# Performance work log

Measured on AMD Instinct MI355X. Metric: run time of the kernel, lower is better.

Reference implementation:

```python
import jax, jax.numpy as jnp
import numpy as np

NUM_PERSISTENT = 16
ALIBI_ALPHA = 1.0
START_I = 0
DILATION = 1
LN_EPS = 1e-5


def setup_inputs() -> dict:
    key = jax.random.key(0)
    ks = jax.random.split(key, 16)
    B, S, C, H = 8, 1024, 512, 8
    D = C // H
    P = NUM_PERSISTENT
    Kk = 3
    x = jax.random.normal(ks[0], (B, S, C), dtype=jnp.float32)
    mask = jnp.ones((B, 1, S, S), dtype=jnp.int32)
    sc = 0.02
    Wq = jax.random.normal(ks[1], (D, D), jnp.float32) * sc
    Wk = jax.random.normal(ks[2], (D, D), jnp.float32) * sc
    Wv = jax.random.normal(ks[3], (D, D), jnp.float32) * sc
    pk = jax.random.normal(ks[4], (P, H, D), jnp.float32) * sc
    pv = jax.random.normal(ks[5], (P, H, D), jnp.float32) * sc
    th_pre = jax.random.normal(ks[6], (H, H), jnp.float32) * (1.0 / np.sqrt(H))
    th_post = jax.random.normal(ks[7], (H, H), jnp.float32) * (1.0 / np.sqrt(H))
    fc_w = jax.random.normal(ks[8], (C, C), jnp.float32) * sc
    fc_b = jnp.zeros((C,), jnp.float32)
    conv1_w = jax.random.normal(ks[9], (C, C, Kk), jnp.float32) * 0.01
    conv1_b = jnp.zeros((C,), jnp.float32)
    conv2_w = jax.random.normal(ks[10], (C, C, Kk), jnp.float32) * 0.01
    conv2_b = jnp.zeros((C,), jnp.float32)
    ln_g = jnp.ones((C,), jnp.float32)
    ln_b = jnp.zeros((C,), jnp.float32)
    return dict(x=x, mask=mask, Wq=Wq, Wk=Wk, Wv=Wv, pk=pk, pv=pv,
                th_pre=th_pre, th_post=th_post, fc_w=fc_w, fc_b=fc_b,
                conv1_w=conv1_w, conv1_b=conv1_b, conv2_w=conv2_w,
                conv2_b=conv2_b, ln_g=ln_g, ln_b=ln_b)


def _causal_conv(x_nct, w_oik, b_o, dilation):
    # padding (k-1)*d on both sides + chomp right == pad left only
    k = w_oik.shape[-1]
    p = (k - 1) * dilation
    y = jax.lax.conv_general_dilated(
        x_nct, w_oik, window_strides=(1,), padding=[(p, 0)],
        rhs_dilation=(dilation,), dimension_numbers=("NCH", "OIH", "NCH"))
    return y + b_o[None, :, None]


def reference(x, mask, Wq, Wk, Wv, pk, pv, th_pre, th_post, fc_w, fc_b,
              conv1_w, conv1_b, conv2_w, conv2_b, ln_g, ln_b):
    N, S, C = x.shape
    H = th_pre.shape[0]
    D = C // H
    P = pk.shape[0]

    # ---- MultiHeadAttention (eval: dropout = identity) ----
    xh = x.reshape(N, S, H, D)
    q = jnp.einsum("nshd,ed->nshe", xh, Wq)
    k = jnp.einsum("nshd,ed->nshe", xh, Wk)
    v = jnp.einsum("nshd,ed->nshe", xh, Wv)
    # persistent memory tokens appended along key/value length
    k = jnp.concatenate([k, jnp.broadcast_to(pk[None], (N, P, H, D))], axis=1)
    v = jnp.concatenate([v, jnp.broadcast_to(pv[None], (N, P, H, D))], axis=1)

    energy = jnp.einsum("nqhd,nkhd->nhqk", q, k)  # (N,H,S,S+P)

    # ALiBi bias (symmetric |q-k|), zero over persistent keys
    slopes = 2.0 ** (-(ALIBI_ALPHA * (jnp.arange(1, H + 1, dtype=jnp.float32) + START_I)))
    t = jnp.arange(S, dtype=jnp.float32)
    dist = jnp.abs(t[:, None] - t[None, :])  # (S,S)
    bias = -dist[None, None] * slopes[None, :, None, None]  # (1,H,S,S)
    bias = jnp.pad(bias, ((0, 0), (0, 0), (0, 0), (0, P)))
    energy = energy + bias

    # pre-softmax talking heads (1x1 conv over head axis)
    energy = jnp.einsum("hg,ngqk->nhqk", th_pre, energy)

    ext_mask = jnp.pad(mask, ((0, 0), (0, 0), (0, 0), (0, P)), constant_values=1)
    energy = jnp.where(ext_mask == 0, jnp.float32(-1e4), energy)

    attn = jax.nn.softmax(energy / jnp.sqrt(jnp.float32(C)), axis=-1)
    attn = jnp.einsum("hg,ngqk->nhqk", th_post, attn)

    att_out = jnp.einsum("nhql,nlhd->nqhd", attn, v).reshape(N, S, C)
    att_out = att_out @ fc_w.T + fc_b

    x = x + att_out  # residual (dropout1 identity in eval)

    # ---- TemporalBlock (causal dilated convs, no SE since heads>0) ----
    xc = jnp.transpose(x, (0, 2, 1))  # (N,C,S)
    h = jax.nn.relu(_causal_conv(xc, conv1_w, conv1_b, DILATION))
    h = jax.nn.relu(_causal_conv(h, conv2_w, conv2_b, DILATION))
    out = jax.nn.relu(h + xc)  # downsample is None (in==out)

    # mask out invalid frames
    conv_mask = mask[:, 0, :, 0][:, None, :]  # (N,1,S)
    out = jnp.where(conv_mask == 0, 0.0, out)

    y = jnp.transpose(out, (0, 2, 1))  # (N,S,C)
    mu = jnp.mean(y, axis=-1, keepdims=True)
    var = jnp.mean(jnp.square(y - mu), axis=-1, keepdims=True)
    y = (y - mu) * jax.lax.rsqrt(var + LN_EPS) * ln_g + ln_b
    return y
```

## Files before the change

kernel.cpp:

```cpp
#include <hip/hip_runtime.h>
#include <hip/hip_bf16.h>

#define BN 8
#define SS 1024
#define CC 512
#define HH 8
#define DD 64
#define PP 16
#define KT 1040
#define KTE 1088

typedef __hip_bfloat16 bf16;
typedef unsigned char uchar;
typedef unsigned short ushort;
typedef unsigned int uint;
typedef __attribute__((ext_vector_type(8))) short short8;
typedef __attribute__((ext_vector_type(4))) float f32x4;
typedef __attribute__((ext_vector_type(2))) float f32x2;

__device__ __forceinline__ short f2s(float v){ bf16 b = __float2bfloat16(v); return *(short*)&b; }
__device__ __forceinline__ float s2f(short s){ bf16 b; *(short*)&b = s; return __bfloat162float(b); }
__device__ __forceinline__ uchar f2q(float v){
    return (uchar)__builtin_amdgcn_cvt_pk_fp8_f32(v, v, 0, false);
}
__device__ __forceinline__ float rfl(float x){
    return __int_as_float(__builtin_amdgcn_readfirstlane(__float_as_int(x)));
}

#define MFMA16(a,b,c)  __builtin_amdgcn_mfma_f32_16x16x32_bf16(a,b,c,0,0,0)
#define MFMAF8(a,b,c)  __builtin_amdgcn_mfma_f32_16x16x32_fp8_fp8(a,b,c,0,0,0)

__global__ __launch_bounds__(256) void prep_kernel(
    const float* __restrict__ fc_w, const float* __restrict__ c1w,
    const float* __restrict__ c2w, const float* __restrict__ Wq,
    const float* __restrict__ Wk, const float* __restrict__ Wv,
    const float* __restrict__ th_post,
    const float* __restrict__ pk, const float* __restrict__ pv,
    short* __restrict__ Bfc, uchar* __restrict__ Bc1,
    uchar* __restrict__ Bc2, short* __restrict__ Bqkv,
    uchar* __restrict__ kf, uchar* __restrict__ vt)
{
    int i = blockIdx.x*256 + threadIdx.x;
    const int NFC = 512*512, NCV = 512*1536, NQ = 3*64*64, NP = BN*HH*PP*DD;
    if (i < NFC) {
        int c = i >> 9, r = i & 511;
        int g = r >> 6, d = r & 63;
        float s = 0.f;
        #pragma unroll
        for (int h = 0; h < 8; ++h)
            s += fc_w[(size_t)c*512 + h*64 + d] * th_post[h*8 + g];
        Bfc[i] = f2s(s);
        return;
    }
    i -= NFC;
    if (i < NCV) {
        int o = i/1536, r = i%1536, dk = r>>9, ci = r&511;
        Bc1[i] = f2q(c1w[(o*512+ci)*3+dk] * 16.f); return;
    }
    i -= NCV;
    if (i < NCV) {
        int o = i/1536, r = i%1536, dk = r>>9, ci = r&511;
        Bc2[i] = f2q(c2w[(o*512+ci)*3+dk] * 16.f); return;
    }
    i -= NCV;
    if (i < NQ) {
        int w = i >> 12, rest = i & 4095;
        const float* W = (w==0)?Wq:(w==1)?Wk:Wv;
        Bqkv[i] = f2s(W[((rest>>6)&63)*64 + (rest&63)]);
        return;
    }
    i -= NQ;
    if (i < NP) {
        int d = i & 63, p = (i >> 6) & 15, h = (i >> 10) & 7, n = i >> 13;
        size_t src = ((size_t)p*HH + h)*DD + d;
        kf[(((size_t)(n*HH+h))*KT + SS + p)*DD + d] = f2q(pk[src]);
        vt[(((size_t)(n*HH+h))*DD + d)*KT + SS + p] = f2q(pv[src]);
    }
}

__global__ __launch_bounds__(256) void qkv_mfma(
    const float* __restrict__ x, const short* __restrict__ Bqkv,
    uchar* __restrict__ qf, uchar* __restrict__ kf, uchar* __restrict__ vt)
{
    __shared__ short Xs[64*72];
    __shared__ short Ws[192*72];
    const int tid = threadIdx.x;
    const int lin = blockIdx.x;
    const int xcd = lin & 7, slot = lin >> 3;
    const int m0 = (xcd*16 + (slot & 15))*64;
    const int h = slot >> 4;
    const int wave = tid >> 6, lane = tid & 63;
    const int lr = lane & 15, lq = lane >> 4;

    for (int i = tid; i < 1024; i += 256) {
        int r = i >> 4, cg = (i & 15)*4;
        float4 v = *(const float4*)(x + (size_t)(m0+r)*CC + h*64 + cg);
        Xs[r*72+cg+0] = f2s(v.x); Xs[r*72+cg+1] = f2s(v.y);
        Xs[r*72+cg+2] = f2s(v.z); Xs[r*72+cg+3] = f2s(v.w);
    }
    for (int i = tid; i < 3072; i += 256) {
        int r = i >> 4, cg = (i & 15)*4;
        *(short4*)(Ws + r*72 + cg) = *(const short4*)(Bqkv + (size_t)r*64 + cg);
    }
    __syncthreads();

    f32x4 acc[12];
    #pragma unroll
    for (int nt = 0; nt < 12; ++nt) acc[nt] = {0.f,0.f,0.f,0.f};
    #pragma unroll
    for (int ks = 0; ks < 2; ++ks) {
        int ko = ks*32 + lq*8;
        short8 a = *(const short8*)(Xs + (wave*16 + lr)*72 + ko);
        #pragma unroll
        for (int nt = 0; nt < 12; ++nt) {
            short8 b = *(const short8*)(Ws + (nt*16 + lr)*72 + ko);
            acc[nt] = MFMA16(a, b, acc[nt]);
        }
    }
    #pragma unroll
    for (int nt = 0; nt < 12; ++nt) {
        int ep = nt*16 + lr;
        int w = ep >> 6, e = ep & 63;
        #pragma unroll
        for (int reg = 0; reg < 4; ++reg) {
            int m = m0 + wave*16 + lq*4 + reg;
            int n = m >> 10, s = m & 1023;
            float v = acc[nt][reg];
            if (w == 0)      qf[((size_t)(n*HH+h)*SS + s)*DD + e] = f2q(v);
            else if (w == 1) kf[((size_t)(n*HH+h)*KT + s)*DD + e] = f2q(v);
            else             vt[(((size_t)(n*HH+h))*DD + e)*KT + s] = f2q(v);
        }
    }
}

__device__ __forceinline__ void en_loadK(const uchar* __restrict__ kf,
    int nh, int kt, int tid, uint2* rk)
{
    #pragma unroll
    for (int j = 0; j < 2; ++j) {
        int i = tid + j*256;
        int r = i >> 3, c8 = (i & 7)*8;
        int kcol = kt*64 + r;
        uint2 v = {0u, 0u};
        if (kcol < KT)
            v = *(const uint2*)(kf + ((size_t)nh*KT + kcol)*DD + c8);
        rk[j] = v;
    }
}

__global__ __launch_bounds__(256) void energy_mfma8(
    const uchar* __restrict__ qf, const uchar* __restrict__ kf,
    uchar* __restrict__ E)
{
    __shared__ uchar Qs[64*72];
    __shared__ uchar Ks[64*72];
    const int tid = threadIdx.x;
    const int lin = blockIdx.x + 16*blockIdx.y;
    const int xcd = lin & 7, slot = lin >> 3;
    const int nh = xcd*8 + (slot & 7);
    const int mt = slot >> 3;
    const int wave = tid >> 6, lane = tid & 63;
    const int lr = lane & 15, lq = lane >> 4;
    const int n = nh >> 3, h = nh & 7;

    #pragma unroll
    for (int j = 0; j < 2; ++j) {
        int i = tid + j*256;
        int r = i >> 3, c8 = (i & 7)*8;
        *(uint2*)(Qs + r*72 + c8) =
            *(const uint2*)(qf + ((size_t)nh*SS + mt*64 + r)*DD + c8);
    }

    uint2 rk[2];
    en_loadK(kf, nh, 0, tid, rk);

    for (int kt = 0; kt < 17; ++kt) {
        if (kt) __syncthreads();
        #pragma unroll
        for (int j = 0; j < 2; ++j) {
            int i = tid + j*256;
            *(uint2*)(Ks + (i >> 3)*72 + (i & 7)*8) = rk[j];
        }
        __syncthreads();
        if (kt + 1 < 17) en_loadK(kf, nh, kt+1, tid, rk);

        f32x4 acc[4];
        #pragma unroll
        for (int nt = 0; nt < 4; ++nt) acc[nt] = {0.f,0.f,0.f,0.f};
        #pragma unroll
        for (int ks = 0; ks < 2; ++ks) {
            int ko = ks*32 + lq*8;
            long a = *(const long*)(Qs + (wave*16 + lr)*72 + ko);
            #pragma unroll
            for (int nt = 0; nt < 4; ++nt) {
                long b = *(const long*)(Ks + (nt*16 + lr)*72 + ko);
                acc[nt] = MFMAF8(a, b, acc[nt]);
            }
        }
        #pragma unroll
        for (int nt = 0; nt < 4; ++nt) {
            int kcol = kt*64 + nt*16 + lr;
            if (kcol >= KT) continue;
            #pragma unroll
            for (int reg = 0; reg < 4; ++reg) {
                int q = mt*64 + wave*16 + lq*4 + reg;
                E[(((size_t)(n*SS + q))*HH + h)*KTE + kcol] = f2q(acc[nt][reg]);
            }
        }
    }
}

__global__ __launch_bounds__(256, 2) void pv_fused(
    const uchar* __restrict__ E, const uchar* __restrict__ vt,
    const int* __restrict__ mask, const float* __restrict__ th_pre,
    short* __restrict__ AO)
{
    __shared__ uchar Ps[4*16*72];
    __shared__ float Sred[16][4];
    const int tid  = threadIdx.x;
    const int n    = blockIdx.x;
    const int yy   = blockIdx.y;
    const int ql0  = (yy >> 1) * 16;
    const int hg   = (yy & 1) * 4;
    const int wave = tid >> 6, lane = tid & 63;
    const int h    = hg + wave;
    const int lr = lane & 15, lq = lane >> 4;
    const int q_l = lane >> 2, kc = lane & 3;
    const int q  = ql0 + q_l;
    const int kcol0 = kc*16;

    const float sc = 0.044194173824159216f * 1.4426950408889634f;
    float tw[8], slmix, shf;
    {
        const float slv[8] = {0.5f,0.25f,0.125f,0.0625f,
                              0.03125f,0.015625f,0.0078125f,0.00390625f};
        const float maxd = (float)((q > SS-1-q) ? q : (SS-1-q));
        float sm = 0.f;
        #pragma unroll
        for (int g = 0; g < 8; ++g) {
            float v = rfl(th_pre[h*8+g] * sc);
            tw[g] = v;
            sm += v * slv[g];
        }
        slmix = rfl(sm);
        shf = fmaxf(0.f, -slmix * maxd);
    }

    const uchar* Eb  = E  + ((size_t)(n*SS + q))*HH*KTE;
    const uchar* Vh  = vt + ((size_t)(n*HH) + h)*DD*KT;
    const int*  mrow = mask + (size_t)n*SS*SS + (size_t)q*SS;
    uchar* Psh = Ps + wave*1152;

    float sums = 0.f;
    f32x4 acc[4];
    #pragma unroll
    for (int j = 0; j < 4; ++j) acc[j] = {0.f,0.f,0.f,0.f};

    for (int kt = 0; kt < 17; ++kt) {
        const int kb = kt*64;
        const bool body = (kt < 16);

        uint4 rE[8];
        #pragma unroll
        for (int g = 0; g < 8; ++g)
            rE[g] = *(const uint4*)(Eb + (size_t)g*KTE + kb + kcol0);
        long bva[2][4];
        #pragma unroll
        for (int ks = 0; ks < 2; ++ks)
            #pragma unroll
            for (int nt = 0; nt < 4; ++nt)
                bva[ks][nt] = *(const long*)(Vh + (size_t)(nt*16+lr)*KT + kb + ks*32 + lq*8);
        int4 rm[4];
        if (body) {
            #pragma unroll
            for (int j = 0; j < 4; ++j)
                rm[j] = *(const int4*)(mrow + kb + kcol0 + j*4);
        }

        #pragma unroll
        for (int s = 0; s < 2; ++s) {
            const int k0 = kb + kcol0 + s*8;
            const bool valid = (k0 < KT);
            f32x4 tA, tB;
            if (body) {
                const float qv = (float)q, kf0 = (float)k0;
                f32x4 dA, dB;
                dA.x = fabsf(qv-kf0);      dA.y = fabsf(qv-kf0-1.f);
                dA.z = fabsf(qv-kf0-2.f);  dA.w = fabsf(qv-kf0-3.f);
                dB.x = fabsf(qv-kf0-4.f);  dB.y = fabsf(qv-kf0-5.f);
                dB.z = fabsf(qv-kf0-6.f);  dB.w = fabsf(qv-kf0-7.f);
                tA = -dA*slmix - shf;
                tB = -dB*slmix - shf;
            } else {
                tA = {-shf,-shf,-shf,-shf};
                tB = tA;
            }
            #pragma unroll
            for (int g = 0; g < 8; ++g) {
                const uint w0 = (s == 0) ? rE[g].x : rE[g].z;
                const uint w1 = (s == 0) ? rE[g].y : rE[g].w;
                f32x2 lo0 = __builtin_amdgcn_cvt_pk_f32_fp8((int)w0, false);
                f32x2 hi0 = __builtin_amdgcn_cvt_pk_f32_fp8((int)w0, true);
                f32x2 lo1 = __builtin_amdgcn_cvt_pk_f32_fp8((int)w1, false);
                f32x2 hi1 = __builtin_amdgcn_cvt_pk_f32_fp8((int)w1, true);
                f32x4 aA; aA.x=lo0.x; aA.y=lo0.y; aA.z=hi0.x; aA.w=hi0.y;
                f32x4 aB; aB.x=lo1.x; aB.y=lo1.y; aB.z=hi1.x; aB.w=hi1.y;
                tA += aA * tw[g];
                tB += aB * tw[g];
            }
            f32x4 eA, eB;
            if (body) {
                const int4 rmA = rm[2*s], rmB = rm[2*s+1];
                eA.x = (rmA.x==0)?0.f:exp2f(tA.x);
                eA.y = (rmA.y==0)?0.f:exp2f(tA.y);
                eA.z = (rmA.z==0)?0.f:exp2f(tA.z);
                eA.w = (rmA.w==0)?0.f:exp2f(tA.w);
                eB.x = (rmB.x==0)?0.f:exp2f(tB.x);
                eB.y = (rmB.y==0)?0.f:exp2f(tB.y);
                eB.z = (rmB.z==0)?0.f:exp2f(tB.z);
                eB.w = (rmB.w==0)?0.f:exp2f(tB.w);
            } else if (valid) {
                eA.x = exp2f(tA.x); eA.y = exp2f(tA.y);
                eA.z = exp2f(tA.z); eA.w = exp2f(tA.w);
                eB.x = exp2f(tB.x); eB.y = exp2f(tB.y);
                eB.z = exp2f(tB.z); eB.w = exp2f(tB.w);
            } else {
                eA = {0.f,0.f,0.f,0.f}; eB = {0.f,0.f,0.f,0.f};
            }
            sums += (eA.x+eA.y)+(eA.z+eA.w) + (eB.x+eB.y)+(eB.z+eB.w);
            int p0 = __builtin_amdgcn_cvt_pk_fp8_f32(eA.x, eA.y, 0, false);
            p0 = __builtin_amdgcn_cvt_pk_fp8_f32(eA.z, eA.w, p0, true);
            int p1 = __builtin_amdgcn_cvt_pk_fp8_f32(eB.x, eB.y, 0, false);
            p1 = __builtin_amdgcn_cvt_pk_fp8_f32(eB.z, eB.w, p1, true);
            uint2 pw; pw.x = (uint)p0; pw.y = (uint)p1;
            *(uint2*)(Psh + q_l*72 + kcol0 + s*8) = pw;
        }

        #pragma unroll
        for (int ks = 0; ks < 2; ++ks) {
            int ko = ks*32 + lq*8;
            long av = *(const long*)(Psh + lr*72 + ko);
            #pragma unroll
            for (int nt = 0; nt < 4; ++nt)
                acc[nt] = MFMAF8(av, bva[ks][nt], acc[nt]);
        }
    }

    {
        float s = sums;
        s += __shfl_xor(s, 1); s += __shfl_xor(s, 2);
        if (kc == 0) Sred[q_l][wave] = 1.0f / s;
    }

    #pragma unroll
    for (int reg = 0; reg < 4; ++reg) {
        float inv = Sred[lq*4 + reg][wave];
        int qg = ql0 + lq*4 + reg;
        #pragma unroll
        for (int nt = 0; nt < 4; ++nt) {
            int d = nt*16 + lr;
            AO[((size_t)(n*SS) + qg)*CC + h*64 + d] = f2s(acc[nt][reg] * inv);
        }
    }
}

__device__ __forceinline__ void g_load4(const short* __restrict__ src,
    size_t rowstride, int row0, int col0, int tid, short4* r)
{
    #pragma unroll
    for (int j = 0; j < 4; ++j) {
        int i = tid + j*256;
        int rr = i >> 4, cg = (i & 15)*4;
        r[j] = *(const short4*)(src + (size_t)(row0 + rr)*rowstride + col0 + cg);
    }
}
__device__ __forceinline__ void lds_store4(short* __restrict__ dst,
    int tid, const short4* r)
{
    #pragma unroll
    for (int j = 0; j < 4; ++j) {
        int i = tid + j*256;
        *(short4*)(dst + (i >> 4)*72 + (i & 15)*4) = r[j];
    }
}

__global__ __launch_bounds__(256) void fc_mfma(
    const short* __restrict__ A, const short* __restrict__ Bt,
    const float* __restrict__ bias, const float* __restrict__ x,
    short* __restrict__ out, uchar* __restrict__ out8)
{
    __shared__ short As[64*72];
    __shared__ short Bs[64*72];
    const int tid = threadIdx.x;
    const int lin = blockIdx.x + 8*blockIdx.y;
    const int xcd = lin & 7, slot = lin >> 3;
    const int m0 = (xcd*16 + (slot & 15))*64;
    const int n0 = (slot >> 4)*64;
    const int wave = tid >> 6, lane = tid & 63;
    const int lr = lane & 15, lq = lane >> 4;

    short4 ra[4], rb[4];
    g_load4(A, CC, m0, 0, tid, ra);
    g_load4(Bt, CC, n0, 0, tid, rb);

    f32x4 acc[4];
    #pragma unroll
    for (int nt = 0; nt < 4; ++nt) acc[nt] = {0.f,0.f,0.f,0.f};

    for (int kt = 0; kt < CC; kt += 64) {
        if (kt) __syncthreads();
        lds_store4(As, tid, ra);
        lds_store4(Bs, tid, rb);
        __syncthreads();
        if (kt + 64 < CC) {
            g_load4(A, CC, m0, kt+64, tid, ra);
            g_load4(Bt, CC, n0, kt+64, tid, rb);
        }
        #pragma unroll
        for (int ks = 0; ks < 2; ++ks) {
            int ko = ks*32 + lq*8;
            short8 a = *(const short8*)(As + (wave*16 + lr)*72 + ko);
            #pragma unroll
            for (int nt = 0; nt < 4; ++nt) {
                short8 b = *(const short8*)(Bs + (nt*16 + lr)*72 + ko);
                acc[nt] = MFMA16(a, b, acc[nt]);
            }
        }
    }
    #pragma unroll
    for (int nt = 0; nt < 4; ++nt) {
        int nn = n0 + nt*16 + lr;
        #pragma unroll
        for (int reg = 0; reg < 4; ++reg) {
            int m = m0 + wave*16 + lq*4 + reg;
            float v = acc[nt][reg] + bias[nn] + x[(size_t)m*CC + nn];
            out[(size_t)m*CC + nn]  = f2s(v);
            out8[(size_t)m*CC + nn] = f2q(v);
        }
    }
}

__device__ __forceinline__ void conv_loadA8w(const uchar* __restrict__ A,
    int m0, int kt, int tid, uint2* ra)
{
    const int shift = (kt >> 9) - 2;
    const int ci0 = kt & 511;
    #pragma unroll
    for (int j = 0; j < 4; ++j) {
        int i = tid + j*256;
        int rr = i >> 4, c8 = (i & 15)*8;
        int m = m0 + rr;
        int s = m & (SS-1);
        uint2 v = {0u, 0u};
        if (s + shift >= 0)
            v = *(const uint2*)(A + (size_t)(m + shift)*CC + ci0 + c8);
        ra[j] = v;
    }
}
__device__ __forceinline__ void g_load8w(const uchar* __restrict__ src,
    size_t rowstride, int row0, int col0, int tid, uint2* r)
{
    #pragma unroll
    for (int j = 0; j < 4; ++j) {
        int i = tid + j*256;
        int rr = i >> 4, c8 = (i & 15)*8;
        r[j] = *(const uint2*)(src + (size_t)(row0 + rr)*rowstride + col0 + c8);
    }
}
__device__ __forceinline__ void lds_store8w(uchar* __restrict__ dst,
    int tid, const uint2* r)
{
    #pragma unroll
    for (int j = 0; j < 4; ++j) {
        int i = tid + j*256;
        *(uint2*)(dst + (i >> 4)*136 + (i & 15)*8) = r[j];
    }
}

__global__ __launch_bounds__(256) void conv_mfma8(
    const uchar* __restrict__ A, const uchar* __restrict__ Bt,
    const float* __restrict__ bias, uchar* __restrict__ out8,
    short* __restrict__ out16, int f8out)
{
    __shared__ uchar As[64*136];
    __shared__ uchar Bs[64*136];
    const int tid = threadIdx.x;
    const int lin = blockIdx.x + 8*blockIdx.y;
    const int xcd = lin & 7, slot = lin >> 3;
    const int m0 = (xcd*16 + (slot & 15))*64;
    const int n0 = (slot >> 4)*64;
    const int wave = tid >> 6, lane = tid & 63;
    const int lr = lane & 15, lq = lane >> 4;

    uint2 ra[4], rb[4];
    conv_loadA8w(A, m0, 0, tid, ra);
    g_load8w(Bt, 1536, n0, 0, tid, rb);

    f32x4 acc[4];
    #pragma unroll
    for (int nt = 0; nt < 4; ++nt) acc[nt] = {0.f,0.f,0.f,0.f};

    for (int kt = 0; kt < 1536; kt += 128) {
        if (kt) __syncthreads();
        lds_store8w(As, tid, ra);
        lds_store8w(Bs, tid, rb);
        __syncthreads();
        if (kt + 128 < 1536) {
            conv_loadA8w(A, m0, kt+128, tid, ra);
            g_load8w(Bt, 1536, n0, kt+128, tid, rb);
        }
        #pragma unroll
        for (int ks = 0; ks < 4; ++ks) {
            int ko = ks*32 + lq*8;
            long a = *(const long*)(As + (wave*16 + lr)*136 + ko);
            #pragma unroll
            for (int nt = 0; nt < 4; ++nt) {
                long b = *(const long*)(Bs + (nt*16 + lr)*136 + ko);
                acc[nt] = MFMAF8(a, b, acc[nt]);
            }
        }
    }
    #pragma unroll
    for (int nt = 0; nt < 4; ++nt) {
        int nn = n0 + nt*16 + lr;
        #pragma unroll
        for (int reg = 0; reg < 4; ++reg) {
            int m = m0 + wave*16 + lq*4 + reg;
            float v = fmaxf(acc[nt][reg]*0.0625f + bias[nn], 0.f);
            if (f8out) out8[(size_t)m*CC + nn]  = f2q(v);
            else       out16[(size_t)m*CC + nn] = f2s(v);
        }
    }
}

__global__ __launch_bounds__(256) void final_kernel(
    const short* __restrict__ c2, const short* __restrict__ xres,
    const int* __restrict__ mask, const float* __restrict__ g,
    const float* __restrict__ b, float* __restrict__ out)
{
    __shared__ float red[256];
    const int tid = threadIdx.x;
    const int m0 = blockIdx.x * 4;
    const int c0 = tid*2;
    const float2 gg = *(const float2*)(g + c0);
    const float2 bb = *(const float2*)(b + c0);

    for (int rr = 0; rr < 4; ++rr) {
        const int m = m0 + rr;
        const int n = m >> 10, s = m & 1023;
        const int mk = mask[(size_t)n*SS*SS + (size_t)s*SS];

        short2 ca = *(const short2*)(c2 + (size_t)m*CC + c0);
        short2 xa = *(const short2*)(xres + (size_t)m*CC + c0);
        float v0 = fmaxf(s2f(ca.x) + s2f(xa.x), 0.f);
        float v1 = fmaxf(s2f(ca.y) + s2f(xa.y), 0.f);
        if (mk == 0) { v0 = 0.f; v1 = 0.f; }

        red[tid] = v0 + v1;
        __syncthreads();
        for (int off = 128; off > 0; off >>= 1) {
            if (tid < off) red[tid] += red[tid + off];
            __syncthreads();
        }
        float mu = red[0] * (1.0f/512.0f);
        __syncthreads();
        float d0 = v0 - mu, d1 = v1 - mu;
        red[tid] = d0*d0 + d1*d1;
        __syncthreads();
        for (int off = 128; off > 0; off >>= 1) {
            if (tid < off) red[tid] += red[tid + off];
            __syncthreads();
        }
        float rstd = rsqrtf(red[0] * (1.0f/512.0f) + 1e-5f);
        float2 o;
        o.x = d0*rstd*gg.x + bb.x;
        o.y = d1*rstd*gg.y + bb.y;
        *(float2*)(out + (size_t)m*CC + c0) = o;
        __syncthreads();
    }
}

extern "C" void kernel_launch(void* const* d_in, const int* in_sizes, int n_in,
                              void* d_out, int out_size, void* d_ws, size_t ws_size,
                              hipStream_t stream)
{
    const float* x      = (const float*)d_in[0];
    const int*   mask   = (const int*)  d_in[1];
    const float* Wq     = (const float*)d_in[2];
    const float* Wk     = (const float*)d_in[3];
    const float* Wv     = (const float*)d_in[4];
    const float* pk     = (const float*)d_in[5];
    const float* pv     = (const float*)d_in[6];
    const float* th_pre = (const float*)d_in[7];
    const float* th_post= (const float*)d_in[8];
    const float* fc_w   = (const float*)d_in[9];
    const float* fc_b   = (const float*)d_in[10];
    const float* c1w    = (const float*)d_in[11];
    const float* c1b    = (const float*)d_in[12];
    const float* c2w    = (const float*)d_in[13];
    const float* c2b    = (const float*)d_in[14];
    const float* lng    = (const float*)d_in[15];
    const float* lnb    = (const float*)d_in[16];
    float* out = (float*)d_out;
    (void)in_sizes; (void)n_in; (void)out_size; (void)ws_size;

    char* ws = (char*)d_ws;
    const size_t SZ_Q  = (size_t)BN*HH*SS*DD;
    const size_t SZ_K  = (size_t)BN*HH*KT*DD;
    const size_t SZ_VT = (size_t)BN*HH*DD*KT;
    const size_t SZ_E  = (size_t)BN*SS*HH*KTE;
    const size_t SZ_A  = (size_t)BN*SS*CC*2;
    const size_t SZ_A8 = (size_t)BN*SS*CC;

    uchar* qf  = (uchar*)(ws);
    uchar* kf  = (uchar*)(ws + SZ_Q);
    uchar* vt  = (uchar*)(ws + SZ_Q + SZ_K);
    uchar* E   = (uchar*)(ws + SZ_Q + SZ_K + SZ_VT);
    short* AO  = (short*)(ws + SZ_Q + SZ_K + SZ_VT + SZ_E);
    char*  wend = ws + SZ_Q + SZ_K + SZ_VT + SZ_E + SZ_A;
    short* Bfc = (short*)(wend);
    uchar* Bc1 = (uchar*)(wend + 512*512*2);
    uchar* Bc2 = (uchar*)(wend + 512*512*2 + 512*1536);
    short* Bqkv= (short*)(wend + 512*512*2 + 2*512*1536);
    uchar* xres8 = (uchar*)(wend + 512*512*2 + 2*512*1536 + 3*64*64*2);
    short* c2buf = (short*)(wend + 512*512*2 + 2*512*1536 + 3*64*64*2 + SZ_A8);
    short* xres = (short*)(ws);
    uchar* h18  = (uchar*)E;

    {
        int total = 512*512 + 2*512*1536 + 3*64*64 + BN*HH*PP*DD;
        prep_kernel<<<(total + 255)/256, 256, 0, stream>>>(
            fc_w, c1w, c2w, Wq, Wk, Wv, th_post, pk, pv,
            Bfc, Bc1, Bc2, Bqkv, kf, vt);
    }
    qkv_mfma<<<BN*SS/64*HH, 256, 0, stream>>>(x, Bqkv, qf, kf, vt);

    energy_mfma8<<<dim3(16, 64), 256, 0, stream>>>(qf, kf, E);
    pv_fused<<<dim3(8, 128), 256, 0, stream>>>(E, vt, mask, th_pre, AO);

    fc_mfma<<<dim3(8, 128), 256, 0, stream>>>(AO, Bfc, fc_b, x, xres, xres8);
    conv_mfma8<<<dim3(8, 128), 256, 0, stream>>>(xres8, Bc1, c1b, h18, (short*)nullptr, 1);
    conv_mfma8<<<dim3(8, 128), 256, 0, stream>>>(h18, Bc2, c2b, (uchar*)nullptr, c2buf, 0);
    final_kernel<<<BN*SS/4, 256, 0, stream>>>(c2buf, xres, mask, lng, lnb, out);
}
```

Baseline: 299.3 us.

## Bit-pack attention mask in prep and prefetch next energy tile in pv_fused

The prep kernel now packs the int32 mask into one bit per key and writes it to a new workspace buffer, so pv_fused reads 32 bits per 32 keys instead of 32 int32 values. pv_fused also software-pipelines its loads, fetching the next tile's energy values and mask word while the current tile is being processed. Together these cut mask bandwidth in the attention-value stage and aim to hide load latency, at the cost of more registers in a kernel launched with a two-blocks-per-SM bound. The int32 mask is still read once, now inside prep.

```diff
diff --git a/kernel.cpp b/kernel.cpp
--- a/kernel.cpp
+++ b/kernel.cpp
@@ -36,12 +36,15 @@
     const float* __restrict__ Wk, const float* __restrict__ Wv,
     const float* __restrict__ th_post,
     const float* __restrict__ pk, const float* __restrict__ pv,
+    const int* __restrict__ mask,
     short* __restrict__ Bfc, uchar* __restrict__ Bc1,
     uchar* __restrict__ Bc2, short* __restrict__ Bqkv,
-    uchar* __restrict__ kf, uchar* __restrict__ vt)
+    uchar* __restrict__ kf, uchar* __restrict__ vt,
+    uint* __restrict__ pm)
 {
     int i = blockIdx.x*256 + threadIdx.x;
     const int NFC = 512*512, NCV = 512*1536, NQ = 3*64*64, NP = BN*HH*PP*DD;
+    const int NM = BN*SS*32;
     if (i < NFC) {
         int c = i >> 9, r = i & 511;
         int g = r >> 6, d = r & 63;
@@ -75,6 +78,22 @@
         size_t src = ((size_t)p*HH + h)*DD + d;
         kf[(((size_t)(n*HH+h))*KT + SS + p)*DD + d] = f2q(pk[src]);
         vt[(((size_t)(n*HH+h))*DD + d)*KT + SS + p] = f2q(pv[src]);
+        return;
+    }
+    i -= NP;
+    if (i < NM) {
+        int w = i & 31, q = (i >> 5) & 1023, n = i >> 15;
+        const int* mr = mask + ((size_t)n*SS + q)*SS + w*32;
+        uint bits = 0;
+        #pragma unroll
+        for (int j = 0; j < 8; ++j) {
+            int4 m = *(const int4*)(mr + j*4);
+            bits |= (m.x != 0 ? 1u : 0u) << (j*4 + 0);
+            bits |= (m.y != 0 ? 1u : 0u) << (j*4 + 1);
+            bits |= (m.z != 0 ? 1u : 0u) << (j*4 + 2);
+            bits |= (m.w != 0 ? 1u : 0u) << (j*4 + 3);
+        }
+        pm[(size_t)(n*SS + q)*32 + w] = bits;
     }
 }
 
@@ -212,7 +231,7 @@
 
 __global__ __launch_bounds__(256, 2) void pv_fused(
     const uchar* __restrict__ E, const uchar* __restrict__ vt,
-    const int* __restrict__ mask, const float* __restrict__ th_pre,
+    const uint* __restrict__ pm, const float* __restrict__ th_pre,
     short* __restrict__ AO)
 {
     __shared__ uchar Ps[4*16*72];
@@ -228,6 +247,7 @@
     const int q_l = lane >> 2, kc = lane & 3;
     const int q  = ql0 + q_l;
     const int kcol0 = kc*16;
+    const int mshift = (kc & 1)*16;
 
     const float sc = 0.044194173824159216f * 1.4426950408889634f;
     float tw[8], slmix, shf;
@@ -248,8 +268,14 @@
 
     const uchar* Eb  = E  + ((size_t)(n*SS + q))*HH*KTE;
     const uchar* Vh  = vt + ((size_t)(n*HH) + h)*DD*KT;
-    const int*  mrow = mask + (size_t)n*SS*SS + (size_t)q*SS;
+    const uint* pmrow = pm + (size_t)(n*SS + q)*32;
     uchar* Psh = Ps + wave*1152;
+
+    uint4 rE[8];
+    #pragma unroll
+    for (int g = 0; g < 8; ++g)
+        rE[g] = *(const uint4*)(Eb + (size_t)g*KTE + kcol0);
+    uint pmw = pmrow[(kc >> 1)];
 
     float sums = 0.f;
     f32x4 acc[4];
@@ -260,21 +286,20 @@
         const int kb = kt*64;
         const bool body = (kt < 16);
 
-        uint4 rE[8];
-        #pragma unroll
-        for (int g = 0; g < 8; ++g)
-            rE[g] = *(const uint4*)(Eb + (size_t)g*KTE + kb + kcol0);
         long bva[2][4];
         #pragma unroll
         for (int ks = 0; ks < 2; ++ks)
             #pragma unroll
             for (int nt = 0; nt < 4; ++nt)
                 bva[ks][nt] = *(const long*)(Vh + (size_t)(nt*16+lr)*KT + kb + ks*32 + lq*8);
-        int4 rm[4];
-        if (body) {
-            #pragma unroll
-            for (int j = 0; j < 4; ++j)
-                rm[j] = *(const int4*)(mrow + kb + kcol0 + j*4);
+
+        uint4 nE[8]; uint npmw = 0;
+        if (kt < 16) {
+            const int nb = kb + 64 + kcol0;
+            #pragma unroll
+            for (int g = 0; g < 8; ++g)
+                nE[g] = *(const uint4*)(Eb + (size_t)g*KTE + nb);
+            if (kt + 1 < 16) npmw = pmrow[(kt+1)*2 + (kc >> 1)];
         }
 
         #pragma unroll
@@ -310,15 +335,15 @@
             }
             f32x4 eA, eB;
             if (body) {
-                const int4 rmA = rm[2*s], rmB = rm[2*s+1];
-                eA.x = (rmA.x==0)?0.f:exp2f(tA.x);
-                eA.y = (rmA.y==0)?0.f:exp2f(tA.y);
-                eA.z = (rmA.z==0)?0.f:exp2f(tA.z);
-                eA.w = (rmA.w==0)?0.f:exp2f(tA.w);
-                eB.x = (rmB.x==0)?0.f:exp2f(tB.x);
-                eB.y = (rmB.y==0)?0.f:exp2f(tB.y);
-                eB.z = (rmB.z==0)?0.f:exp2f(tB.z);
-                eB.w = (rmB.w==0)?0.f:exp2f(tB.w);
+                const uint bits = (pmw >> (mshift + s*8)) & 0xffu;
+                eA.x = (bits & 0x01u) ? exp2f(tA.x) : 0.f;
+                eA.y = (bits & 0x02u) ? exp2f(tA.y) : 0.f;
+                eA.z = (bits & 0x04u) ? exp2f(tA.z) : 0.f;
+                eA.w = (bits & 0x08u) ? exp2f(tA.w) : 0.f;
+                eB.x = (bits & 0x10u) ? exp2f(tB.x) : 0.f;
+                eB.y = (bits & 0x20u) ? exp2f(tB.y) : 0.f;
+                eB.z = (bits & 0x40u) ? exp2f(tB.z) : 0.f;
+                eB.w = (bits & 0x80u) ? exp2f(tB.w) : 0.f;
             } else if (valid) {
                 eA.x = exp2f(tA.x); eA.y = exp2f(tA.y);
                 eA.z = exp2f(tA.z); eA.w = exp2f(tA.w);
@@ -343,6 +368,12 @@
             #pragma unroll
             for (int nt = 0; nt < 4; ++nt)
                 acc[nt] = MFMAF8(av, bva[ks][nt], acc[nt]);
+        }
+
+        if (kt < 16) {
+            #pragma unroll
+            for (int g = 0; g < 8; ++g) rE[g] = nE[g];
+            pmw = npmw;
         }
     }
 
@@ -624,19 +655,20 @@
     short* Bqkv= (short*)(wend + 512*512*2 + 2*512*1536);
     uchar* xres8 = (uchar*)(wend + 512*512*2 + 2*512*1536 + 3*64*64*2);
     short* c2buf = (short*)(wend + 512*512*2 + 2*512*1536 + 3*64*64*2 + SZ_A8);
+    uint*  pmb   = (uint*) (wend + 512*512*2 + 2*512*1536 + 3*64*64*2 + SZ_A8 + SZ_A);
     short* xres = (short*)(ws);
     uchar* h18  = (uchar*)E;
 
     {
-        int total = 512*512 + 2*512*1536 + 3*64*64 + BN*HH*PP*DD;
+        int total = 512*512 + 2*512*1536 + 3*64*64 + BN*HH*PP*DD + BN*SS*32;
         prep_kernel<<<(total + 255)/256, 256, 0, stream>>>(
-            fc_w, c1w, c2w, Wq, Wk, Wv, th_post, pk, pv,
-            Bfc, Bc1, Bc2, Bqkv, kf, vt);
+            fc_w, c1w, c2w, Wq, Wk, Wv, th_post, pk, pv, mask,
+            Bfc, Bc1, Bc2, Bqkv, kf, vt, pmb);
     }
     qkv_mfma<<<BN*SS/64*HH, 256, 0, stream>>>(x, Bqkv, qf, kf, vt);
 
     energy_mfma8<<<dim3(16, 64), 256, 0, stream>>>(qf, kf, E);
-    pv_fused<<<dim3(8, 128), 256, 0, stream>>>(E, vt, mask, th_pre, AO);
+    pv_fused<<<dim3(8, 128), 256, 0, stream>>>(E, vt, pmb, th_pre, AO);
 
     fc_mfma<<<dim3(8, 128), 256, 0, stream>>>(AO, Bfc, fc_b, x, xres, xres8);
     conv_mfma8<<<dim3(8, 128), 256, 0, stream>>>(xres8, Bc1, c1b, h18, (short*)nullptr, 1);
```

Result: no change. 296.5 us (-0.9%).
